# Performance work log

Measured on AMD Instinct MI355X. Metric: run time of the kernel, lower is better.

The kernel has to match this reference:

```python
import jax, jax.numpy as jnp
import numpy as np
from jax import lax

# ---- geometry (from Mamba2PoSTMixer defaults + chosen d_model) ----
D_MODEL = 1024
EXPAND = 2
HEADDIM = 64
D_STATE = 128
D_CONV = 4
CHUNK = 256
D_INNER = EXPAND * D_MODEL            # 2048
NHEADS = D_INNER // HEADDIM           # 32
D_CONV_CH = D_INNER + 2 * D_STATE     # conv acts on x, B, C
D_IN_PROJ = 2 * D_INNER + 2 * D_STATE + NHEADS
BATCH, SEQLEN = 2, 4096
EPS = 1e-5


def setup_inputs() -> dict:
    key = jax.random.key(0)
    ks = jax.random.split(key, 8)
    f = jnp.float32
    return {
        "hidden_states": jax.random.normal(ks[0], (BATCH, SEQLEN, D_MODEL), f),
        "residual": jax.random.normal(ks[1], (BATCH, SEQLEN, D_MODEL), f),
        "norm_weight": jnp.ones((D_MODEL,), f),
        "in_proj_w": jax.random.normal(ks[2], (D_MODEL, D_IN_PROJ), f) * 0.02,
        "conv_w": jax.random.normal(ks[3], (D_CONV, 1, D_CONV_CH), f) * 0.2,  # WIO, depthwise
        "conv_b": jnp.zeros((D_CONV_CH,), f),
        "dt_bias": jnp.log(jnp.expm1(jax.random.uniform(ks[4], (NHEADS,), f, 1e-3, 1e-1))),
        "A_log": jnp.log(jax.random.uniform(ks[5], (NHEADS,), f, 1.0, 16.0)),
        "D": jnp.ones((NHEADS,), f),
        "gate_norm_weight": jnp.ones((D_INNER,), f),
        "out_proj_w": jax.random.normal(ks[6], (D_INNER, D_MODEL), f) * 0.02,
    }


def _rmsnorm(x, w, eps=EPS):
    return x * lax.rsqrt(jnp.mean(x * x, axis=-1, keepdims=True) + eps) * w


def _segsum(x):
    # x: [..., T] -> [..., T, T] lower-triangular cumulative segment sums
    T = x.shape[-1]
    cs = jnp.cumsum(x, axis=-1)
    ss = cs[..., :, None] - cs[..., None, :]
    mask = jnp.tril(jnp.ones((T, T), bool))
    return jnp.where(mask, ss, -jnp.inf)


def _ssd(xdt, dtA, Bm, Cm):
    # xdt: [b,l,h,p] (x already scaled by dt), dtA: [b,l,h], Bm/Cm: [b,l,n]
    b, l, h, p = xdt.shape
    n = Bm.shape[-1]
    c = l // CHUNK
    x = xdt.reshape(b, c, CHUNK, h, p)
    A = dtA.reshape(b, c, CHUNK, h).transpose(0, 3, 1, 2)     # [b,h,c,l]
    Bc = Bm.reshape(b, c, CHUNK, n)
    Cc = Cm.reshape(b, c, CHUNK, n)
    A_cum = jnp.cumsum(A, axis=-1)                            # [b,h,c,l]
    # intra-chunk (diagonal block) output
    L = jnp.exp(_segsum(A))                                   # [b,h,c,l,s]
    Y_diag = jnp.einsum('bcln,bcsn,bhcls,bcshp->bclhp', Cc, Bc, L, x)
    # per-chunk final states
    decay_states = jnp.exp(A_cum[..., -1:] - A_cum)           # [b,h,c,l]
    states = jnp.einsum('bcln,bhcl,bclhp->bchpn', Bc, decay_states, x)
    # inter-chunk recurrence over chunk states
    chunk_decay = jnp.exp(A_cum[..., -1])                     # [b,h,c]
    def step(carry, inp):
        dec, s = inp                                          # dec: [b,h], s: [b,h,p,n]
        return carry * dec[..., None, None] + s, carry
    init = jnp.zeros((b, h, p, n), xdt.dtype)
    _, prev = lax.scan(step, init,
                       (jnp.moveaxis(chunk_decay, -1, 0), jnp.moveaxis(states, 1, 0)))
    prev = jnp.moveaxis(prev, 0, 1)                           # [b,c,h,p,n] states entering each chunk
    Y_off = jnp.einsum('bcln,bchpn,bhcl->bclhp', Cc, prev, jnp.exp(A_cum))
    return (Y_diag + Y_off).reshape(b, l, h, p)


def reference(hidden_states, residual, norm_weight, in_proj_w, conv_w, conv_b,
              dt_bias, A_log, D, gate_norm_weight, out_proj_w):
    # residual add + RMSNorm (Mamba2PoSTBlock)
    res = hidden_states + residual
    h = _rmsnorm(res, norm_weight)
    # Mamba2 mixer
    zxbcdt = h @ in_proj_w                                    # [b,l, 2*Di + 2*N + H]
    z, xBC, dt_raw = jnp.split(zxbcdt, [D_INNER, D_INNER + D_CONV_CH], axis=-1)
    # depthwise causal conv over (x, B, C) channels + SiLU
    xp = jnp.pad(xBC, ((0, 0), (D_CONV - 1, 0), (0, 0)))
    xBC = lax.conv_general_dilated(xp, conv_w, (1,), 'VALID',
                                   dimension_numbers=('NWC', 'WIO', 'NWC'),
                                   feature_group_count=D_CONV_CH) + conv_b
    xBC = jax.nn.silu(xBC)
    x, Bm, Cm = jnp.split(xBC, [D_INNER, D_INNER + D_STATE], axis=-1)
    dt = jax.nn.softplus(dt_raw + dt_bias)                    # [b,l,H]
    A = -jnp.exp(A_log)                                       # [H]
    xh = x.reshape(x.shape[0], x.shape[1], NHEADS, HEADDIM)   # [b,l,h,p]
    y = _ssd(xh * dt[..., None], dt * A, Bm, Cm)
    y = y + D[None, None, :, None] * xh                       # skip (D) term
    y = y.reshape(y.shape[0], y.shape[1], D_INNER)
    y = _rmsnorm(y * jax.nn.silu(z), gate_norm_weight)        # gated RMSNorm
    out = y @ out_proj_w
    return out, res
```

## Files before the change

kernel.cpp:

```cpp
#include <hip/hip_runtime.h>
#include <hip/hip_bf16.h>
#include <math.h>

#define BATCH   2
#define LQ      4096
#define RTOT    8192
#define DM      1024
#define DI      2048
#define NH      32
#define HD      64
#define DS      128
#define CH      256
#define NC      16
#define XBC_C   2304
#define ZX_C    4384
#define ZXS     4352
#define NP1     4608
#define EPS     1e-5f
#define LOG2E   1.4426950408889634f

typedef __hip_bfloat16 bf16;
typedef __bf16 bf16x8v __attribute__((ext_vector_type(8)));
typedef __bf16 bf16x4v __attribute__((ext_vector_type(4)));
typedef float f32x4v __attribute__((ext_vector_type(4)));

#define CSWZ(row, col) ((col) ^ ((((row) >> 3) & 7) << 3))

__device__ __forceinline__ float block_reduce_sum(float v) {
    __shared__ float sred[8];
    int lane = threadIdx.x & 63, w = threadIdx.x >> 6;
#pragma unroll
    for (int off = 32; off > 0; off >>= 1) v += __shfl_down(v, off, 64);
    if (lane == 0) sred[w] = v;
    __syncthreads();
    float t = (threadIdx.x < (int)(blockDim.x >> 6)) ? sred[threadIdx.x] : 0.f;
    if (w == 0) {
#pragma unroll
        for (int off = 4; off > 0; off >>= 1) t += __shfl_down(t, off, 64);
        if (lane == 0) sred[0] = t;
    }
    __syncthreads();
    return sred[0];
}

__device__ __forceinline__ void transpose_tile(
    const float* __restrict__ W, bf16* __restrict__ WT, int K, int N,
    int n0, int k0) {
    __shared__ float t[32][33];
    int tx = threadIdx.x & 31, ty = threadIdx.x >> 5;
#pragma unroll
    for (int r = 0; r < 32; r += 8) {
        int k = k0 + ty + r, n = n0 + tx;
        t[ty + r][tx] = (n < N) ? W[(size_t)k * N + n] : 0.f;
    }
    __syncthreads();
#pragma unroll
    for (int r = 0; r < 32; r += 8) {
        int n = n0 + ty + r, k = k0 + tx;
        WT[(size_t)n * K + k] = __float2bfloat16(t[tx][ty + r]);
    }
}

__global__ __launch_bounds__(256) void fused_pre_kernel(
    const float* __restrict__ hid, const float* __restrict__ resid,
    const float* __restrict__ w, float* __restrict__ res_out,
    bf16* __restrict__ h_out, const float* __restrict__ in_proj,
    bf16* __restrict__ Bt1) {
    int bid = blockIdx.x;
    if (bid < RTOT) {
        int r = bid, tid = threadIdx.x;
        size_t base = (size_t)r * DM;
        float4 hv = *(const float4*)&hid[base + tid * 4];
        float4 rv = *(const float4*)&resid[base + tid * 4];
        float4 s = {hv.x + rv.x, hv.y + rv.y, hv.z + rv.z, hv.w + rv.w};
        *(float4*)&res_out[base + tid * 4] = s;
        float ss = s.x * s.x + s.y * s.y + s.z * s.z + s.w * s.w;
        ss = block_reduce_sum(ss);
        float scale = rsqrtf(ss / (float)DM + EPS);
        float4 wv = *(const float4*)&w[tid * 4];
        __hip_bfloat162 p0, p1;
        p0.x = __float2bfloat16(s.x * scale * wv.x);
        p0.y = __float2bfloat16(s.y * scale * wv.y);
        p1.x = __float2bfloat16(s.z * scale * wv.z);
        p1.y = __float2bfloat16(s.w * scale * wv.w);
        bf16* hp = &h_out[base + tid * 4];
        *(__hip_bfloat162*)hp = p0;
        *(__hip_bfloat162*)(hp + 2) = p1;
    } else {
        int t = bid - RTOT;
        transpose_tile(in_proj, Bt1, DM, ZX_C, (t % 144) * 32, (t / 144) * 32);
    }
}

#define GFENCE asm volatile("" ::: "memory")
#define GBAR do { GFENCE; __builtin_amdgcn_s_barrier(); GFENCE; } while (0)
#define GWAIT_LGKM                                                             \
    do {                                                                       \
        asm volatile("s_waitcnt lgkmcnt(0)" ::: "memory");                     \
        __builtin_amdgcn_sched_barrier(0);                                     \
    } while (0)
#define GWAIT_VM0 asm volatile("s_waitcnt vmcnt(0)" ::: "memory")
#define GWAIT_VMN                                                              \
    do {                                                                       \
        if constexpr (BN == 256)                                               \
            asm volatile("s_waitcnt vmcnt(6)" ::: "memory");                   \
        else                                                                   \
            asm volatile("s_waitcnt vmcnt(4)" ::: "memory");                   \
    } while (0)

#define RD_A(buf, ml)                                                          \
    do {                                                                       \
        _Pragma("unroll") for (int mt_ = 0; mt_ < 4; ++mt_)                    \
        _Pragma("unroll") for (int kk_ = 0; kk_ < 2; ++kk_)                    \
            aF[mt_][kk_] = *(const bf16x8v*)&As[buf][                          \
                (wm * 128 + ((ml) * 4 + mt_) * 16 + fr) * 64 +                 \
                ((((kk_ << 2) | kg) ^ s7) << 3)];                              \
    } while (0)

#define RD_B(buf)                                                              \
    do {                                                                       \
        _Pragma("unroll") for (int nt_ = 0; nt_ < NTW; ++nt_)                  \
        _Pragma("unroll") for (int kk_ = 0; kk_ < 2; ++kk_)                    \
            bF[nt_][kk_] = *(const bf16x8v*)&Bs[buf][                          \
                (wn * (BN / 4) + nt_ * 16 + fr) * 64 +                         \
                ((((kk_ << 2) | kg) ^ s7) << 3)];                              \
    } while (0)

#define QMFMA(ml, nl)                                                          \
    do {                                                                       \
        __builtin_amdgcn_s_setprio(1);                                         \
        _Pragma("unroll") for (int mt_ = 0; mt_ < 4; ++mt_)                    \
        _Pragma("unroll") for (int nt_ = 0; nt_ < NTH; ++nt_)                  \
        _Pragma("unroll") for (int kk_ = 0; kk_ < 2; ++kk_)                    \
            acc[(ml) * 4 + mt_][(nl) * NTH + nt_] =                            \
                __builtin_amdgcn_mfma_f32_16x16x32_bf16(                       \
                    aF[mt_][kk_], bF[(nl) * NTH + nt_][kk_],                   \
                    acc[(ml) * 4 + mt_][(nl) * NTH + nt_], 0, 0, 0);           \
        __builtin_amdgcn_s_setprio(0);                                         \
    } while (0)

template <int BN, int WRITE_F32>
__global__ __launch_bounds__(512, 2) void gemm_8ph_kernel(
    const bf16* __restrict__ A, int lda, const bf16* __restrict__ Bt, int ldb,
    void* __restrict__ C, int ldc, int NXT, int K, float* __restrict__ dtraw) {
    constexpr int BM = 256;
    constexpr int NTW = BN / 64;
    constexpr int NTH = NTW / 2;
    constexpr int BLOADS = BN / 128;
    __shared__ __align__(16) bf16 As[2][BM * 64];
    __shared__ __align__(16) bf16 Bs[2][BN * 64];

    const int tid = threadIdx.x;
    const int lane = tid & 63;
    const int wave = tid >> 6;
    const int wm = wave >> 2, wn = wave & 3;
    const int fr = lane & 15, kg = lane >> 4;
    const int s7 = fr & 7;

    const int bid = blockIdx.x;
    const int xcd = bid & 7;
    const int local = bid >> 3;
    const int MPX = ((int)gridDim.x >> 3) / NXT;
    const int mtile = xcd * MPX + (local % MPX);
    const int m0 = mtile * BM;
    const int n0 = (local / MPX) * BN;

    const int trow = tid >> 3;
    const int scol = ((tid & 7) ^ (trow & 7)) << 3;
    const bf16* aSrc = A + (size_t)(m0 + trow) * lda + scol;
    const bf16* bSrc = Bt + (size_t)(n0 + trow) * ldb + scol;

    auto stageA = [&](int kt, int h) {
#pragma unroll
        for (int j = 0; j < 2; ++j)
            __builtin_amdgcn_global_load_lds(
                (const __attribute__((address_space(1))) void*)(
                    aSrc + (size_t)(h * 128 + j * 64) * lda + kt * 64),
                (__attribute__((address_space(3))) void*)(
                    &As[kt & 1][(h * 128 + j * 64) * 64 + tid * 8]),
                16, 0, 0);
    };
    auto stageB = [&](int kt, int h) {
#pragma unroll
        for (int j = 0; j < BLOADS; ++j)
            __builtin_amdgcn_global_load_lds(
                (const __attribute__((address_space(1))) void*)(
                    bSrc + (size_t)(h * (BN / 2) + j * 64) * ldb + kt * 64),
                (__attribute__((address_space(3))) void*)(
                    &Bs[kt & 1][(h * (BN / 2) + j * 64) * 64 + tid * 8]),
                16, 0, 0);
    };

    f32x4v acc[8][NTW] = {};
    bf16x8v aF[4][2], bF[NTW][2];

    stageB(0, 0); stageB(0, 1); stageA(0, 0); stageA(0, 1);
    stageB(1, 0); stageB(1, 1); stageA(1, 0);
    GWAIT_VMN;
    GBAR;

    const int NIT = K >> 7;
    for (int t = 0; t < NIT; ++t) {
        const int k1 = 2 * t + 1, k2 = 2 * t + 2, k3 = 2 * t + 3;
        const bool full = (t < NIT - 1);
        RD_B(0); RD_A(0, 0);
        stageA(k1, 1);
        GBAR; GWAIT_LGKM;
        QMFMA(0, 0);
        GBAR;
        if (full) stageB(k2, 0);
        GBAR;
        QMFMA(0, 1);
        GBAR;
        RD_A(0, 1);
        if (full) stageB(k2, 1);
        GBAR; GWAIT_LGKM;
        QMFMA(1, 0);
        GBAR;
        if (full) stageA(k2, 0);
        GBAR;
        QMFMA(1, 1);
        if (full) { GWAIT_VMN; } else { GWAIT_VM0; }
        GBAR;
        RD_B(1); RD_A(1, 0);
        if (full) stageA(k2, 1);
        GBAR; GWAIT_LGKM;
        QMFMA(0, 0);
        GBAR;
        if (full) stageB(k3, 0);
        GBAR;
        QMFMA(0, 1);
        GBAR;
        RD_A(1, 1);
        if (full) stageB(k3, 1);
        GBAR; GWAIT_LGKM;
        QMFMA(1, 0);
        GBAR;
        if (full) stageA(k3, 0);
        GBAR;
        QMFMA(1, 1);
        if (full) { GWAIT_VMN; }
        GBAR;
    }

#pragma unroll
    for (int mt = 0; mt < 8; ++mt) {
#pragma unroll
        for (int nt = 0; nt < NTW; ++nt) {
            int gn = n0 + wn * (BN / 4) + nt * 16 + fr;
#pragma unroll
            for (int rg = 0; rg < 4; ++rg) {
                int gm = m0 + wm * 128 + mt * 16 + kg * 4 + rg;
                float v = acc[mt][nt][rg];
                if (WRITE_F32) {
                    ((float*)C)[(size_t)gm * ldc + gn] = v;
                } else {
                    if (gn < 4352)
                        ((bf16*)C)[(size_t)gm * ldc + gn] = __float2bfloat16(v);
                    else if (gn < 4384)
                        dtraw[(size_t)gm * 32 + (gn - 4352)] = v;
                }
            }
        }
    }
}

__global__ __launch_bounds__(256) void fused_conv_dt_kernel(
    const bf16* __restrict__ zx, const float* __restrict__ conv_w,
    const float* __restrict__ conv_b, bf16* __restrict__ xBC,
    const float* __restrict__ dtraw, const float* __restrict__ dt_bias,
    const float* __restrict__ A_log, float* __restrict__ dt_bh,
    float* __restrict__ Ac2_bh) {
    int bid = blockIdx.x;
    if (bid < 9216) {
        int idx = bid * 256 + threadIdx.x;
        int r = idx / 288;
        int o = idx - r * 288;
        int c = o * 8;
        int b = r >> 12, l = r & (LQ - 1);
        float acc[8];
        {
            float4 cb0 = *(const float4*)&conv_b[c];
            float4 cb1 = *(const float4*)&conv_b[c + 4];
            acc[0] = cb0.x; acc[1] = cb0.y; acc[2] = cb0.z; acc[3] = cb0.w;
            acc[4] = cb1.x; acc[5] = cb1.y; acc[6] = cb1.z; acc[7] = cb1.w;
        }
#pragma unroll
        for (int k = 0; k < 4; ++k) {
            int t = l - 3 + k;
            if (t >= 0) {
                bf16x8v xv = *(const bf16x8v*)&zx[(size_t)(b * LQ + t) * ZXS + DI + c];
                float4 w0 = *(const float4*)&conv_w[k * XBC_C + c];
                float4 w1 = *(const float4*)&conv_w[k * XBC_C + c + 4];
                acc[0] = fmaf(w0.x, (float)xv[0], acc[0]);
                acc[1] = fmaf(w0.y, (float)xv[1], acc[1]);
                acc[2] = fmaf(w0.z, (float)xv[2], acc[2]);
                acc[3] = fmaf(w0.w, (float)xv[3], acc[3]);
                acc[4] = fmaf(w1.x, (float)xv[4], acc[4]);
                acc[5] = fmaf(w1.y, (float)xv[5], acc[5]);
                acc[6] = fmaf(w1.z, (float)xv[6], acc[6]);
                acc[7] = fmaf(w1.w, (float)xv[7], acc[7]);
            }
        }
        bf16x8v ov;
#pragma unroll
        for (int j = 0; j < 8; ++j)
            ov[j] = (__bf16)(acc[j] / (1.f + __expf(-acc[j])));
        *(bf16x8v*)&xBC[(size_t)r * XBC_C + c] = ov;
    } else {
        __shared__ float sA[256];
        int b2 = bid - 9216;
        int c = b2 & 15, h = (b2 >> 4) & 31, b = b2 >> 9;
        int tid = threadIdx.x;
        int l = c * CH + tid;
        int r = b * LQ + l;
        float v = dtraw[(size_t)r * 32 + h] + dt_bias[h];
        float dt = (v > 20.f) ? v : log1pf(expf(v));
        float A = -expf(A_log[h]);
        sA[tid] = dt * A * LOG2E;
        __syncthreads();
        for (int off = 1; off < 256; off <<= 1) {
            float t = (tid >= off) ? sA[tid - off] : 0.f;
            __syncthreads();
            sA[tid] += t;
            __syncthreads();
        }
        size_t o = (size_t)(b * NH + h) * LQ + l;
        dt_bh[o] = dt;
        Ac2_bh[o] = sA[tid];
    }
}

__global__ __launch_bounds__(256) void states_mfma_kernel(
    const bf16* __restrict__ xBC, const float* __restrict__ dt_bh,
    const float* __restrict__ Ac2, float* __restrict__ states) {
    __shared__ __align__(16) __bf16 xdT[64][264];
    __shared__ __align__(16) __bf16 BT[64][264];
    int bid = blockIdx.x;
    int c = bid & 15, h = (bid >> 4) & 31, b = bid >> 9;
    int bh = b * NH + h;
    int rch = b * LQ + c * CH;
    int tid = threadIdx.x;
    int wave = tid >> 6, lane = tid & 63;
    int fr = lane & 15, kg = lane >> 4;
    float Ac2last = Ac2[(size_t)bh * LQ + c * CH + (CH - 1)];

    {
        int p2 = (tid & 31) * 2;
        int srow = tid >> 5;
        int key = ((p2 >> 3) & 7) << 3;
#pragma unroll 4
        for (int pass = 0; pass < 32; ++pass) {
            int s = pass * 8 + srow;
            float sc = dt_bh[(size_t)bh * LQ + c * CH + s] *
                       exp2f(Ac2last - Ac2[(size_t)bh * LQ + c * CH + s]);
            __hip_bfloat162 xv =
                *(const __hip_bfloat162*)&xBC[(size_t)(rch + s) * XBC_C + h * HD + p2];
            int sx = s ^ key;
            xdT[p2][sx]     = (__bf16)(__bfloat162float(xv.x) * sc);
            xdT[p2 + 1][sx] = (__bf16)(__bfloat162float(xv.y) * sc);
        }
    }
    int wm = (wave >> 1) * 32, wn = (wave & 1) * 32;
    size_t base = (size_t)(bh * NC + c) * HD * DS;
    for (int nh = 0; nh < 2; ++nh) {
        __syncthreads();
        {
            int n_oct = tid & 7, lrow = tid >> 3;
#pragma unroll
            for (int pass = 0; pass < 8; ++pass) {
                int l = pass * 32 + lrow;
                int lx = l ^ (n_oct << 3);
                bf16x8v bv = *(const bf16x8v*)
                    &xBC[(size_t)(rch + l) * XBC_C + DI + nh * 64 + n_oct * 8];
#pragma unroll
                for (int j = 0; j < 8; ++j)
                    BT[n_oct * 8 + j][lx] = bv[j];
            }
        }
        __syncthreads();
        f32x4v acc[2][2] = {};
#pragma unroll
        for (int kb = 0; kb < 8; ++kb) {
            bf16x8v A2[2], B2[2];
#pragma unroll
            for (int i = 0; i < 2; ++i) {
                int row = wm + i * 16 + fr;
                A2[i] = *(const bf16x8v*)&xdT[row][CSWZ(row, kb * 32 + kg * 8)];
            }
#pragma unroll
            for (int j = 0; j < 2; ++j) {
                int row = wn + j * 16 + fr;
                B2[j] = *(const bf16x8v*)&BT[row][CSWZ(row, kb * 32 + kg * 8)];
            }
#pragma unroll
            for (int i = 0; i < 2; ++i)
#pragma unroll
                for (int j = 0; j < 2; ++j)
                    acc[i][j] = __builtin_amdgcn_mfma_f32_16x16x32_bf16(
                        A2[i], B2[j], acc[i][j], 0, 0, 0);
        }
#pragma unroll
        for (int i = 0; i < 2; ++i)
#pragma unroll
            for (int j = 0; j < 2; ++j)
#pragma unroll
                for (int rg = 0; rg < 4; ++rg) {
                    int p = wm + i * 16 + kg * 4 + rg;
                    int n = nh * 64 + wn + j * 16 + fr;
                    states[base + (size_t)p * DS + n] = acc[i][j][rg];
                }
    }
}

__global__ __launch_bounds__(256) void chunk_scan_kernel(
    float* __restrict__ states, const float* __restrict__ Ac2) {
    int bh = blockIdx.x >> 3;
    int sl = blockIdx.x & 7;
    int tid = threadIdx.x;
    float carry[4];
#pragma unroll
    for (int j = 0; j < 4; ++j) carry[j] = 0.f;
    for (int c = 0; c < NC; ++c) {
        float dec = exp2f(Ac2[(size_t)bh * LQ + c * CH + (CH - 1)]);
        size_t base = (size_t)(bh * NC + c) * (HD * DS) + sl * 1024;
#pragma unroll
        for (int j = 0; j < 4; ++j) {
            size_t idx = base + tid + j * 256;
            float tmp = states[idx];
            states[idx] = carry[j];
            carry[j] = carry[j] * dec + tmp;
        }
    }
}

template <int MASKED>
__device__ __forceinline__ void y_slab(
    const bf16* __restrict__ xBC, int rch, int s0, int fr, int kg,
    const float* As_sh, const float* Al, const bf16x8v CA[4][4],
    __bf16 (*Pw)[36], const __bf16 (*xdtT)[264], f32x4v accY[4][4]) {
#pragma unroll
    for (int half = 0; half < 2; ++half) {
        f32x4v Sacc[2][4] = {};
#pragma unroll
        for (int ks = 0; ks < 4; ++ks) {
            bf16x8v SB[2];
#pragma unroll
            for (int st2 = 0; st2 < 2; ++st2)
                SB[st2] = *(const bf16x8v*)&xBC[
                    (size_t)(rch + s0 + half * 32 + st2 * 16 + fr) * XBC_C
                    + DI + ks * 32 + kg * 8];
#pragma unroll
            for (int st2 = 0; st2 < 2; ++st2)
#pragma unroll
                for (int mt = 0; mt < 4; ++mt) {
                    if (MASKED && (half * 2 + st2) > mt) continue;
                    Sacc[st2][mt] = __builtin_amdgcn_mfma_f32_16x16x32_bf16(
                        SB[st2], CA[mt][ks], Sacc[st2][mt], 0, 0, 0);
                }
        }
#pragma unroll
        for (int st2 = 0; st2 < 2; ++st2) {
            int sblk = half * 2 + st2;
            float4 As4 = *(const float4*)&As_sh[s0 + half * 32 + st2 * 16 + kg * 4];
            float as[4] = {As4.x, As4.y, As4.z, As4.w};
#pragma unroll
            for (int mt = 0; mt < 4; ++mt) {
                bf16x4v pv;
                if (MASKED && sblk > mt) {
                    pv[0] = pv[1] = pv[2] = pv[3] = (__bf16)0.f;
                } else {
#pragma unroll
                    for (int rg = 0; rg < 4; ++rg) {
                        float v = Sacc[st2][mt][rg] * exp2f(Al[mt] - as[rg]);
                        if (MASKED && sblk == mt && (kg * 4 + rg) > fr) v = 0.f;
                        pv[rg] = (__bf16)v;
                    }
                }
                *(bf16x4v*)&Pw[mt * 16 + fr][st2 * 16 + kg * 4] = pv;
            }
        }
        __asm__ volatile("s_waitcnt lgkmcnt(0)" ::: "memory");
        bf16x8v PA[4], XB[4];
#pragma unroll
        for (int mt = 0; mt < 4; ++mt) {
            bf16x4v plo = *(const bf16x4v*)&Pw[mt * 16 + fr][kg * 8];
            bf16x4v phi = *(const bf16x4v*)&Pw[mt * 16 + fr][kg * 8 + 4];
            bf16x8v pa;
#pragma unroll
            for (int j = 0; j < 4; ++j) { pa[j] = plo[j]; pa[4 + j] = phi[j]; }
            PA[mt] = pa;
        }
#pragma unroll
        for (int pt = 0; pt < 4; ++pt) {
            int row = pt * 16 + fr;
            XB[pt] = *(const bf16x8v*)&xdtT[row][
                CSWZ(row, s0 + half * 32 + kg * 8)];
        }
#pragma unroll
        for (int mt = 0; mt < 4; ++mt)
#pragma unroll
            for (int pt = 0; pt < 4; ++pt)
                accY[mt][pt] = __builtin_amdgcn_mfma_f32_16x16x32_bf16(
                    PA[mt], XB[pt], accY[mt][pt], 0, 0, 0);
        __asm__ volatile("s_waitcnt lgkmcnt(0)" ::: "memory");
    }
}

__global__ __launch_bounds__(256) void y_mfma_kernel(
    const bf16* __restrict__ xBC, const float* __restrict__ dt_bh,
    const float* __restrict__ Ac2, const float* __restrict__ prev,
    bf16* __restrict__ yout ) {
    __shared__ __align__(16) __bf16 xdtT[64][264];
    __shared__ __align__(16) __bf16 P[4][64][36];
    __shared__ float As_sh[256];
    int bid = blockIdx.x;
    int c = bid & 15, h = (bid >> 4) & 31, b = bid >> 9;
    int bh = b * NH + h;
    int rch = b * LQ + c * CH;
    int tid = threadIdx.x;
    int wave = tid >> 6, lane = tid & 63;
    int fr = lane & 15, kg = lane >> 4;

    As_sh[tid] = Ac2[(size_t)bh * LQ + c * CH + tid];
    {
        int p2 = (tid & 31) * 2;
        int srow = tid >> 5;
        int key = ((p2 >> 3) & 7) << 3;
#pragma unroll 4
        for (int pass = 0; pass < 32; ++pass) {
            int s = pass * 8 + srow;
            float dtv = dt_bh[(size_t)bh * LQ + c * CH + s];
            __hip_bfloat162 xv =
                *(const __hip_bfloat162*)&xBC[(size_t)(rch + s) * XBC_C + h * HD + p2];
            int sx = s ^ key;
            xdtT[p2][sx]     = (__bf16)(__bfloat162float(xv.x) * dtv);
            xdtT[p2 + 1][sx] = (__bf16)(__bfloat162float(xv.y) * dtv);
        }
    }
    __syncthreads();

    bf16x8v CA[4][4];
    {
        size_t rb = (size_t)(rch + wave * 64 + fr) * XBC_C + DI + DS + kg * 8;
#pragma unroll
        for (int mt = 0; mt < 4; ++mt)
#pragma unroll
            for (int ks = 0; ks < 4; ++ks)
                CA[mt][ks] = *(const bf16x8v*)&xBC[rb + (size_t)mt * 16 * XBC_C + ks * 32];
    }

    f32x4v accY[4][4] = {};

    {
        size_t pbase = (size_t)(bh * NC + c) * HD * DS;
#pragma unroll
        for (int ks = 0; ks < 4; ++ks) {
            bf16x8v PB[4];
#pragma unroll
            for (int pt = 0; pt < 4; ++pt) {
                const float* pp = &prev[pbase + (size_t)(pt * 16 + fr) * DS + ks * 32 + kg * 8];
                float4 a4 = *(const float4*)pp;
                float4 b4 = *(const float4*)(pp + 4);
                bf16x8v t;
                t[0] = (__bf16)a4.x; t[1] = (__bf16)a4.y; t[2] = (__bf16)a4.z; t[3] = (__bf16)a4.w;
                t[4] = (__bf16)b4.x; t[5] = (__bf16)b4.y; t[6] = (__bf16)b4.z; t[7] = (__bf16)b4.w;
                PB[pt] = t;
            }
#pragma unroll
            for (int mt = 0; mt < 4; ++mt)
#pragma unroll
                for (int pt = 0; pt < 4; ++pt)
                    accY[mt][pt] = __builtin_amdgcn_mfma_f32_16x16x32_bf16(
                        CA[mt][ks], PB[pt], accY[mt][pt], 0, 0, 0);
        }
    }
    int l0 = wave * 64;
#pragma unroll
    for (int mt = 0; mt < 4; ++mt) {
#pragma unroll
        for (int rg = 0; rg < 4; ++rg) {
            float e = exp2f(As_sh[l0 + mt * 16 + kg * 4 + rg]);
#pragma unroll
            for (int pt = 0; pt < 4; ++pt)
                accY[mt][pt][rg] *= e;
        }
    }

    float Al[4];
#pragma unroll
    for (int mt = 0; mt < 4; ++mt) Al[mt] = As_sh[l0 + mt * 16 + fr];

    __bf16 (*Pw)[36] = P[wave];
    for (int st = 0; st < wave; ++st)
        y_slab<0>(xBC, rch, st * 64, fr, kg, As_sh, Al, CA, Pw, xdtT, accY);
    y_slab<1>(xBC, rch, l0, fr, kg, As_sh, Al, CA, Pw, xdtT, accY);

#pragma unroll
    for (int ph = 0; ph < 2; ++ph) {
#pragma unroll
        for (int mt = 0; mt < 4; ++mt)
#pragma unroll
            for (int ptl = 0; ptl < 2; ++ptl)
#pragma unroll
                for (int rg = 0; rg < 4; ++rg)
                    Pw[mt * 16 + kg * 4 + rg][ptl * 16 + fr] =
                        (__bf16)accY[mt][ph * 2 + ptl][rg];
        __asm__ volatile("s_waitcnt lgkmcnt(0)" ::: "memory");
        bf16* yp = yout + (size_t)(rch + l0 + lane) * ZXS + h * HD + ph * 32;
#pragma unroll
        for (int q = 0; q < 4; ++q) {
            bf16x4v a = *(const bf16x4v*)&Pw[lane][q * 8];
            bf16x4v bq = *(const bf16x4v*)&Pw[lane][q * 8 + 4];
            bf16x8v v;
#pragma unroll
            for (int j = 0; j < 4; ++j) { v[j] = a[j]; v[4 + j] = bq[j]; }
            *(bf16x8v*)(yp + q * 8) = v;
        }
        __asm__ volatile("s_waitcnt lgkmcnt(0)" ::: "memory");
    }
}

__global__ __launch_bounds__(256) void fused_gate_trans_kernel(
    const bf16* __restrict__ zx, const float* __restrict__ gw,
    const float* __restrict__ Dvec, const bf16* __restrict__ xBC,
    bf16* __restrict__ y ,
    const float* __restrict__ out_proj, bf16* __restrict__ Bt2) {
    int bid = blockIdx.x;
    if (bid < RTOT) {
        int r = bid, tid = threadIdx.x;
        int i0 = tid * 8;
        bf16x8v zv = *(const bf16x8v*)&zx[(size_t)r * ZXS + i0];
        bf16x8v yv = *(const bf16x8v*)&y[(size_t)r * ZXS + i0];
        bf16x8v xv = *(const bf16x8v*)&xBC[(size_t)r * XBC_C + i0];
        float Dh = Dvec[tid >> 3];
        float v[8];
        float ss = 0.f;
#pragma unroll
        for (int j = 0; j < 8; ++j) {
            float z = (float)zv[j];
            float val = ((float)yv[j] + Dh * (float)xv[j]) * (z / (1.f + __expf(-z)));
            v[j] = val;
            ss += val * val;
        }
        ss = block_reduce_sum(ss);
        float scale = rsqrtf(ss / (float)DI + EPS);
        float4 g0 = *(const float4*)&gw[i0];
        float4 g1 = *(const float4*)&gw[i0 + 4];
        float g[8] = {g0.x, g0.y, g0.z, g0.w, g1.x, g1.y, g1.z, g1.w};
        bf16x8v ov;
#pragma unroll
        for (int j = 0; j < 8; ++j)
            ov[j] = (__bf16)(v[j] * scale * g[j]);
        *(bf16x8v*)&y[(size_t)r * ZXS + i0] = ov;
    } else {
        int t = bid - RTOT;
        transpose_tile(out_proj, Bt2, DI, DM, (t & 31) * 32, (t >> 5) * 32);
    }
}

extern "C" void kernel_launch(void* const* d_in, const int* in_sizes, int n_in,
                              void* d_out, int out_size, void* d_ws, size_t ws_size,
                              hipStream_t stream) {
    const float* hid      = (const float*)d_in[0];
    const float* resid    = (const float*)d_in[1];
    const float* norm_w   = (const float*)d_in[2];
    const float* in_proj  = (const float*)d_in[3];
    const float* conv_w   = (const float*)d_in[4];
    const float* conv_b   = (const float*)d_in[5];
    const float* dt_bias  = (const float*)d_in[6];
    const float* A_log    = (const float*)d_in[7];
    const float* Dvec     = (const float*)d_in[8];
    const float* gate_w   = (const float*)d_in[9];
    const float* out_proj = (const float*)d_in[10];

    float* out_p   = (float*)d_out;
    float* res_out = out_p + (size_t)RTOT * DM;
    bf16*  h_bf16  = (bf16*)out_p;
    float* states  = out_p;

    char* wsb = (char*)d_ws;
    bf16*  zx      = (bf16*)wsb;  wsb += (size_t)RTOT * ZXS * sizeof(bf16);
    bf16*  xBC     = (bf16*)wsb;  wsb += (size_t)RTOT * XBC_C * sizeof(bf16);
    float* dtraw   = (float*)wsb; wsb += (size_t)RTOT * 32 * sizeof(float);
    float* dt_bh   = (float*)wsb; wsb += (size_t)BATCH * NH * LQ * sizeof(float);
    float* Ac2_bh  = (float*)wsb; wsb += (size_t)BATCH * NH * LQ * sizeof(float);
    wsb += (size_t)1 << 20;
    bf16* Bt1 = xBC;
    bf16* Bt2 = (bf16*)dtraw;

    fused_pre_kernel<<<RTOT + 4608, 256, 0, stream>>>(
        hid, resid, norm_w, res_out, h_bf16, in_proj, Bt1);
    gemm_8ph_kernel<256, 0><<<576, 512, 0, stream>>>(
        h_bf16, DM, Bt1, DM, zx, ZXS, 18, DM, dtraw);
    fused_conv_dt_kernel<<<9216 + 1024, 256, 0, stream>>>(
        zx, conv_w, conv_b, xBC, dtraw, dt_bias, A_log, dt_bh, Ac2_bh);
    states_mfma_kernel<<<BATCH * NH * NC, 256, 0, stream>>>(
        xBC, dt_bh, Ac2_bh, states);
    chunk_scan_kernel<<<BATCH * NH * 8, 256, 0, stream>>>(states, Ac2_bh);
    y_mfma_kernel<<<BATCH * NH * NC, 256, 0, stream>>>(
        xBC, dt_bh, Ac2_bh, states, zx + DI);
    fused_gate_trans_kernel<<<RTOT + 2048, 256, 0, stream>>>(
        zx, gate_w, Dvec, xBC, zx + DI, out_proj, Bt2);
    gemm_8ph_kernel<128, 1><<<256, 512, 0, stream>>>(
        zx + DI, ZXS, Bt2, DI, out_p, DM, 8, DI, nullptr);
}
```

Before: 486.8 us.

## Restructure GEMM main loop into per-tile halves with interleaved fragment loads

Replaces the 8-phase GEMM mainloop, which had many block barriers and explicit lgkmcnt waits, with a per-K-tile schedule. A whole A+B tile is staged into the other LDS buffer at the start of each half. LDS fragment reads go into two register banks and are interleaved with MFMA slots, with only sched_barriers between them. Only one block barrier and one full vmcnt(0) wait remain per K-tile. This cuts synchronisation overhead and lets LDS reads overlap with MFMA, but the global prefetch depth is limited to one tile and every half drains all outstanding loads.

```diff
diff --git a/kernel.cpp b/kernel.cpp
--- a/kernel.cpp
+++ b/kernel.cpp
@@ -94,49 +94,60 @@
 
 #define GFENCE asm volatile("" ::: "memory")
 #define GBAR do { GFENCE; __builtin_amdgcn_s_barrier(); GFENCE; } while (0)
-#define GWAIT_LGKM                                                             \
-    do {                                                                       \
-        asm volatile("s_waitcnt lgkmcnt(0)" ::: "memory");                     \
-        __builtin_amdgcn_sched_barrier(0);                                     \
-    } while (0)
 #define GWAIT_VM0 asm volatile("s_waitcnt vmcnt(0)" ::: "memory")
-#define GWAIT_VMN                                                              \
-    do {                                                                       \
-        if constexpr (BN == 256)                                               \
-            asm volatile("s_waitcnt vmcnt(6)" ::: "memory");                   \
-        else                                                                   \
-            asm volatile("s_waitcnt vmcnt(4)" ::: "memory");                   \
-    } while (0)
-
-#define RD_A(buf, ml)                                                          \
+#define SBAR __builtin_amdgcn_sched_barrier(0)
+
+#define ISS_A(bank, mh, k)                                                     \
     do {                                                                       \
         _Pragma("unroll") for (int mt_ = 0; mt_ < 4; ++mt_)                    \
-        _Pragma("unroll") for (int kk_ = 0; kk_ < 2; ++kk_)                    \
-            aF[mt_][kk_] = *(const bf16x8v*)&As[buf][                          \
-                (wm * 128 + ((ml) * 4 + mt_) * 16 + fr) * 64 +                 \
-                ((((kk_ << 2) | kg) ^ s7) << 3)];                              \
+            bank[mt_] = *(const bf16x8v*)&AsB[                                 \
+                (wm * 128 + (mh) * 64 + mt_ * 16 + fr) * 64 +                  \
+                (((((k) << 2) | kg) ^ s7) << 3)];                              \
     } while (0)
 
-#define RD_B(buf)                                                              \
+#define ISS_B(bank, nh, k)                                                     \
     do {                                                                       \
-        _Pragma("unroll") for (int nt_ = 0; nt_ < NTW; ++nt_)                  \
-        _Pragma("unroll") for (int kk_ = 0; kk_ < 2; ++kk_)                    \
-            bF[nt_][kk_] = *(const bf16x8v*)&Bs[buf][                          \
-                (wn * (BN / 4) + nt_ * 16 + fr) * 64 +                         \
-                ((((kk_ << 2) | kg) ^ s7) << 3)];                              \
+        _Pragma("unroll") for (int nt_ = 0; nt_ < NTH; ++nt_)                  \
+            bank[nt_] = *(const bf16x8v*)&BsB[                                 \
+                (wn * (BN / 4) + (nh) * (NTH * 16) + nt_ * 16 + fr) * 64 +     \
+                (((((k) << 2) | kg) ^ s7) << 3)];                              \
     } while (0)
 
-#define QMFMA(ml, nl)                                                          \
+#define MSLOT(mh, nh, AB, BB)                                                  \
     do {                                                                       \
         __builtin_amdgcn_s_setprio(1);                                         \
         _Pragma("unroll") for (int mt_ = 0; mt_ < 4; ++mt_)                    \
         _Pragma("unroll") for (int nt_ = 0; nt_ < NTH; ++nt_)                  \
-        _Pragma("unroll") for (int kk_ = 0; kk_ < 2; ++kk_)                    \
-            acc[(ml) * 4 + mt_][(nl) * NTH + nt_] =                            \
+            acc[(mh) * 4 + mt_][(nh) * NTH + nt_] =                            \
                 __builtin_amdgcn_mfma_f32_16x16x32_bf16(                       \
-                    aF[mt_][kk_], bF[(nl) * NTH + nt_][kk_],                   \
-                    acc[(ml) * 4 + mt_][(nl) * NTH + nt_], 0, 0, 0);           \
+                    AB[mt_], BB[nt_],                                          \
+                    acc[(mh) * 4 + mt_][(nh) * NTH + nt_], 0, 0, 0);           \
         __builtin_amdgcn_s_setprio(0);                                         \
+        SBAR;                                                                  \
+    } while (0)
+
+#define HALF(bufc, doStage, stKt)                                              \
+    do {                                                                       \
+        const bf16* AsB = &As[bufc][0];                                        \
+        const bf16* BsB = &Bs[bufc][0];                                        \
+        if (doStage) stage_tile(stKt);                                         \
+        ISS_A(a0, 0, 0); ISS_B(b0, 0, 0);                           \
+        SBAR;                                                                  \
+        ISS_B(b1, 1, 0);                                            \
+        MSLOT(0, 0, a0, b0);                                           \
+        ISS_A(a1, 0, 1); ISS_B(b0, 0, 1);                           \
+        MSLOT(0, 1, a0, b1);                                           \
+        ISS_B(b1, 1, 1);                                            \
+        MSLOT(0, 0, a1, b0);                                           \
+        ISS_A(a0, 1, 0); ISS_B(b0, 0, 0);                           \
+        MSLOT(0, 1, a1, b1);                                           \
+        ISS_B(b1, 1, 0);                                            \
+        MSLOT(1, 0, a0, b0);                                           \
+        ISS_A(a1, 1, 1); ISS_B(b0, 0, 1);                           \
+        MSLOT(1, 1, a0, b1);                                           \
+        ISS_B(b1, 1, 1);                                            \
+        MSLOT(1, 0, a1, b0);                                           \
+        MSLOT(1, 1, a1, b1);                                           \
     } while (0)
 
 template <int BN, int WRITE_F32>
@@ -146,7 +157,7 @@
     constexpr int BM = 256;
     constexpr int NTW = BN / 64;
     constexpr int NTH = NTW / 2;
-    constexpr int BLOADS = BN / 128;
+    constexpr int BL = BN / 64;
     __shared__ __align__(16) bf16 As[2][BM * 64];
     __shared__ __align__(16) bf16 Bs[2][BN * 64];
 
@@ -170,76 +181,45 @@
     const bf16* aSrc = A + (size_t)(m0 + trow) * lda + scol;
     const bf16* bSrc = Bt + (size_t)(n0 + trow) * ldb + scol;
 
-    auto stageA = [&](int kt, int h) {
-#pragma unroll
-        for (int j = 0; j < 2; ++j)
+    auto stage_tile = [&](int kt) {
+#pragma unroll
+        for (int j = 0; j < 4; ++j)
             __builtin_amdgcn_global_load_lds(
                 (const __attribute__((address_space(1))) void*)(
-                    aSrc + (size_t)(h * 128 + j * 64) * lda + kt * 64),
+                    aSrc + (size_t)(j * 64) * lda + kt * 64),
                 (__attribute__((address_space(3))) void*)(
-                    &As[kt & 1][(h * 128 + j * 64) * 64 + tid * 8]),
+                    &As[kt & 1][j * 64 * 64 + tid * 8]),
+                16, 0, 0);
+#pragma unroll
+        for (int j = 0; j < BL; ++j)
+            __builtin_amdgcn_global_load_lds(
+                (const __attribute__((address_space(1))) void*)(
+                    bSrc + (size_t)(j * 64) * ldb + kt * 64),
+                (__attribute__((address_space(3))) void*)(
+                    &Bs[kt & 1][j * 64 * 64 + tid * 8]),
                 16, 0, 0);
     };
-    auto stageB = [&](int kt, int h) {
-#pragma unroll
-        for (int j = 0; j < BLOADS; ++j)
-            __builtin_amdgcn_global_load_lds(
-                (const __attribute__((address_space(1))) void*)(
-                    bSrc + (size_t)(h * (BN / 2) + j * 64) * ldb + kt * 64),
-                (__attribute__((address_space(3))) void*)(
-                    &Bs[kt & 1][(h * (BN / 2) + j * 64) * 64 + tid * 8]),
-                16, 0, 0);
-    };
 
     f32x4v acc[8][NTW] = {};
-    bf16x8v aF[4][2], bF[NTW][2];
-
-    stageB(0, 0); stageB(0, 1); stageA(0, 0); stageA(0, 1);
-    stageB(1, 0); stageB(1, 1); stageA(1, 0);
-    GWAIT_VMN;
+    bf16x8v a0[4], a1[4];
+    bf16x8v b0[NTH], b1[NTH];
+
+    stage_tile(0);
+    stage_tile(1);
+    if constexpr (BN == 256)
+        asm volatile("s_waitcnt vmcnt(8)" ::: "memory");
+    else
+        asm volatile("s_waitcnt vmcnt(6)" ::: "memory");
     GBAR;
 
-    const int NIT = K >> 7;
-    for (int t = 0; t < NIT; ++t) {
-        const int k1 = 2 * t + 1, k2 = 2 * t + 2, k3 = 2 * t + 3;
-        const bool full = (t < NIT - 1);
-        RD_B(0); RD_A(0, 0);
-        stageA(k1, 1);
-        GBAR; GWAIT_LGKM;
-        QMFMA(0, 0);
+    const int KT = K >> 6;
+    const int NT = KT >> 1;
+    for (int t = 0; t < NT; ++t) {
+        HALF(0, (t > 0), 2 * t + 1);
+        GWAIT_VM0;
         GBAR;
-        if (full) stageB(k2, 0);
-        GBAR;
-        QMFMA(0, 1);
-        GBAR;
-        RD_A(0, 1);
-        if (full) stageB(k2, 1);
-        GBAR; GWAIT_LGKM;
-        QMFMA(1, 0);
-        GBAR;
-        if (full) stageA(k2, 0);
-        GBAR;
-        QMFMA(1, 1);
-        if (full) { GWAIT_VMN; } else { GWAIT_VM0; }
-        GBAR;
-        RD_B(1); RD_A(1, 0);
-        if (full) stageA(k2, 1);
-        GBAR; GWAIT_LGKM;
-        QMFMA(0, 0);
-        GBAR;
-        if (full) stageB(k3, 0);
-        GBAR;
-        QMFMA(0, 1);
-        GBAR;
-        RD_A(1, 1);
-        if (full) stageB(k3, 1);
-        GBAR; GWAIT_LGKM;
-        QMFMA(1, 0);
-        GBAR;
-        if (full) stageA(k3, 0);
-        GBAR;
-        QMFMA(1, 1);
-        if (full) { GWAIT_VMN; }
+        HALF(1, (2 * t + 2 < KT), 2 * t + 2);
+        GWAIT_VM0;
         GBAR;
     }
 
```

After: 491.8 us. Within noise of the previous version (+1.0%).
